# Kernel tuning notes

Hardware: AMD Instinct MI355X
Metric: run time of the kernel (lower is better)

## Reference

```python
import jax, jax.numpy as jnp
import numpy as np

NUM_NODES = 2_000_000
INPUT_DIM = 128
NUM_GRAPHS = 16_384


def setup_inputs() -> dict:
    key = jax.random.key(0)
    k1, k2, k3 = jax.random.split(key, 3)
    x = jax.random.normal(k1, (NUM_NODES, INPUT_DIM), dtype=jnp.float32)
    batch = jnp.sort(jax.random.randint(k2, (NUM_NODES,), 0, NUM_GRAPHS, dtype=jnp.int64))
    # Linear(input_dim, 1) parameters
    W = jax.random.normal(k3, (INPUT_DIM, 1), dtype=jnp.float32) / np.sqrt(INPUT_DIM)
    b = jnp.zeros((1,), dtype=jnp.float32)
    return {"x": x, "batch": batch, "W": W, "b": b}


def reference(x, batch, W, b) -> jnp.ndarray:
    # scores: [N, 1]; softmax over dim=0 (ALL nodes, matching source exactly)
    scores = x @ W + b
    attn = jax.nn.softmax(scores, axis=0)  # [N, 1]
    # weighted features, then scatter-add by graph id (global_add_pool)
    pooled = jax.ops.segment_sum(x * attn, batch, num_segments=NUM_GRAPHS)
    return pooled  # [NUM_GRAPHS, INPUT_DIM]
```

## Files before the change

kernel.cpp:

```cpp
#include <hip/hip_runtime.h>
#include <math.h>

#define N_NODES  2000000
#define DIM      128
#define N_GRAPHS 16384

#define FBLOCKS  2048
#define WAVES    (FBLOCKS * 4)
#define RPW      ((N_NODES + WAVES - 1) / WAVES)

typedef float v4f __attribute__((ext_vector_type(4)));

__global__ __launch_bounds__(256, 8) void fused_kernel(const float* __restrict__ x,
                                                       const int* __restrict__ batch,
                                                       const float* __restrict__ W,
                                                       const float* __restrict__ b,
                                                       float* __restrict__ acc,
                                                       float* __restrict__ blkZ) {
    const int tid  = threadIdx.x;
    const int lane = tid & 63;
    const int l32  = lane & 31;
    const int half = lane >> 5;
    const int wave = blockIdx.x * 4 + (tid >> 6);

    const v4f  wf   = __builtin_nontemporal_load((const v4f*)W + l32);
    const float bias = b[0];

    const int r0 = wave * RPW;
    const int r1 = min(r0 + RPW, N_NODES);

    float zacc = 0.f;

    int r = r0;
    while (r < r1) {
        const int g = batch[r];
        int lo = r + 1, hi = r1;
        while (lo < hi) {
            const int mid = (lo + hi) >> 1;
            if (batch[mid] <= g) lo = mid + 1; else hi = mid;
        }
        const int end = lo;

        v4f racc = {0.f, 0.f, 0.f, 0.f};
        #pragma unroll 4
        for (int rr = r; rr < end; rr += 2) {
            const int row = rr + half;
            if (row < end) {
                const v4f xv = __builtin_nontemporal_load(
                    (const v4f*)(x + (long)row * DIM) + l32);
                float sv = xv[0] * wf[0] + xv[1] * wf[1] + xv[2] * wf[2] + xv[3] * wf[3];
                #pragma unroll
                for (int m = 16; m >= 1; m >>= 1) sv += __shfl_xor(sv, m, 64);
                const float e = __expf(sv + bias);
                zacc += e;
                racc[0] = fmaf(xv[0], e, racc[0]);
                racc[1] = fmaf(xv[1], e, racc[1]);
                racc[2] = fmaf(xv[2], e, racc[2]);
                racc[3] = fmaf(xv[3], e, racc[3]);
            }
        }
        racc[0] += __shfl_xor(racc[0], 32, 64);
        racc[1] += __shfl_xor(racc[1], 32, 64);
        racc[2] += __shfl_xor(racc[2], 32, 64);
        racc[3] += __shfl_xor(racc[3], 32, 64);
        if (half == 0) {
            float* a = acc + (long)g * DIM + l32 * 4;
            atomicAdd(a + 0, racc[0]);
            atomicAdd(a + 1, racc[1]);
            atomicAdd(a + 2, racc[2]);
            atomicAdd(a + 3, racc[3]);
        }
        r = end;
    }

    zacc += __shfl_xor(zacc, 32, 64);
    __shared__ float sm[4];
    if (lane == 0) sm[tid >> 6] = zacc;
    __syncthreads();
    if (tid == 0) blkZ[blockIdx.x] = sm[0] + sm[1] + sm[2] + sm[3];
}

__global__ __launch_bounds__(256) void finalize_kernel(const float* __restrict__ acc,
                                                       const float* __restrict__ blkZ,
                                                       float* __restrict__ out) {
    __shared__ float sm[256];
    float v = 0.f;
    #pragma unroll
    for (int i = 0; i < FBLOCKS / 256; ++i) v += blkZ[i * 256 + threadIdx.x];
    sm[threadIdx.x] = v;
    __syncthreads();
    #pragma unroll
    for (int st = 128; st >= 1; st >>= 1) {
        if (threadIdx.x < st) sm[threadIdx.x] += sm[threadIdx.x + st];
        __syncthreads();
    }
    const float invZ = 1.0f / sm[0];

    const int i = blockIdx.x * 256 + threadIdx.x;
    const float4 a = ((const float4*)acc)[i];
    float4 o;
    o.x = a.x * invZ; o.y = a.y * invZ; o.z = a.z * invZ; o.w = a.w * invZ;
    ((float4*)out)[i] = o;
}

extern "C" void kernel_launch(void* const* d_in, const int* in_sizes, int n_in,
                              void* d_out, int out_size, void* d_ws, size_t ws_size,
                              hipStream_t stream) {
    const float* x     = (const float*)d_in[0];
    const int*   batch = (const int*)d_in[1];
    const float* W     = (const float*)d_in[2];
    const float* b     = (const float*)d_in[3];
    float* out = (float*)d_out;

    float* acc  = (float*)d_ws;
    float* blkZ = acc + (long)N_GRAPHS * DIM;

    hipMemsetAsync(acc, 0, (size_t)N_GRAPHS * DIM * sizeof(float), stream);

    fused_kernel<<<FBLOCKS, 256, 0, stream>>>(x, batch, W, b, acc, blkZ);

    const int fin_grid = (N_GRAPHS * DIM / 4) / 256;
    finalize_kernel<<<fin_grid, 256, 0, stream>>>(acc, blkZ, out);
}
```

Baseline: 196.1 us.

## Assign one wave per graph and drop atomics and memset

Work is now split by graph instead of by equal node ranges. Each wave binary-searches its graph's row range in the sorted batch array, accumulates that graph alone, and writes the result directly to the output. This removes the accumulator memset, the float atomics and the separate accumulator buffer, and the final pass now scales the output in place. In exchange each wave pays two full-array binary searches, and load balance now depends on graph sizes, which are roughly uniform for this input.

```diff
diff --git a/kernel.cpp b/kernel.cpp
--- a/kernel.cpp
+++ b/kernel.cpp
@@ -5,72 +5,65 @@
 #define DIM      128
 #define N_GRAPHS 16384
 
-#define FBLOCKS  2048
-#define WAVES    (FBLOCKS * 4)
-#define RPW      ((N_NODES + WAVES - 1) / WAVES)
+#define GBLOCKS  4096
+#define ZENT     GBLOCKS
 
 typedef float v4f __attribute__((ext_vector_type(4)));
+
+__device__ __forceinline__ int lower_bound(const int* __restrict__ batch, int target) {
+    int lo = 0, hi = N_NODES;
+    while (lo < hi) {
+        const int mid = (lo + hi) >> 1;
+        if (batch[mid] < target) lo = mid + 1; else hi = mid;
+    }
+    return lo;
+}
 
 __global__ __launch_bounds__(256, 8) void fused_kernel(const float* __restrict__ x,
                                                        const int* __restrict__ batch,
                                                        const float* __restrict__ W,
                                                        const float* __restrict__ b,
-                                                       float* __restrict__ acc,
+                                                       float* __restrict__ out,
                                                        float* __restrict__ blkZ) {
     const int tid  = threadIdx.x;
     const int lane = tid & 63;
     const int l32  = lane & 31;
     const int half = lane >> 5;
-    const int wave = blockIdx.x * 4 + (tid >> 6);
+    const int g    = blockIdx.x * 4 + (tid >> 6);
 
-    const v4f  wf   = __builtin_nontemporal_load((const v4f*)W + l32);
+    const v4f wf    = *((const v4f*)W + l32);
     const float bias = b[0];
 
-    const int r0 = wave * RPW;
-    const int r1 = min(r0 + RPW, N_NODES);
+    const int r0 = lower_bound(batch, g);
+    const int r1 = lower_bound(batch, g + 1);
 
     float zacc = 0.f;
+    v4f racc = {0.f, 0.f, 0.f, 0.f};
 
-    int r = r0;
-    while (r < r1) {
-        const int g = batch[r];
-        int lo = r + 1, hi = r1;
-        while (lo < hi) {
-            const int mid = (lo + hi) >> 1;
-            if (batch[mid] <= g) lo = mid + 1; else hi = mid;
+    #pragma unroll 4
+    for (int rr = r0; rr < r1; rr += 2) {
+        const int row = rr + half;
+        if (row < r1) {
+            const v4f xv = __builtin_nontemporal_load(
+                (const v4f*)(x + (long)row * DIM) + l32);
+            float sv = xv[0] * wf[0] + xv[1] * wf[1] + xv[2] * wf[2] + xv[3] * wf[3];
+            #pragma unroll
+            for (int m = 16; m >= 1; m >>= 1) sv += __shfl_xor(sv, m, 64);
+            const float e = __expf(sv + bias);
+            zacc += e;
+            racc[0] = fmaf(xv[0], e, racc[0]);
+            racc[1] = fmaf(xv[1], e, racc[1]);
+            racc[2] = fmaf(xv[2], e, racc[2]);
+            racc[3] = fmaf(xv[3], e, racc[3]);
         }
-        const int end = lo;
+    }
 
-        v4f racc = {0.f, 0.f, 0.f, 0.f};
-        #pragma unroll 4
-        for (int rr = r; rr < end; rr += 2) {
-            const int row = rr + half;
-            if (row < end) {
-                const v4f xv = __builtin_nontemporal_load(
-                    (const v4f*)(x + (long)row * DIM) + l32);
-                float sv = xv[0] * wf[0] + xv[1] * wf[1] + xv[2] * wf[2] + xv[3] * wf[3];
-                #pragma unroll
-                for (int m = 16; m >= 1; m >>= 1) sv += __shfl_xor(sv, m, 64);
-                const float e = __expf(sv + bias);
-                zacc += e;
-                racc[0] = fmaf(xv[0], e, racc[0]);
-                racc[1] = fmaf(xv[1], e, racc[1]);
-                racc[2] = fmaf(xv[2], e, racc[2]);
-                racc[3] = fmaf(xv[3], e, racc[3]);
-            }
-        }
-        racc[0] += __shfl_xor(racc[0], 32, 64);
-        racc[1] += __shfl_xor(racc[1], 32, 64);
-        racc[2] += __shfl_xor(racc[2], 32, 64);
-        racc[3] += __shfl_xor(racc[3], 32, 64);
-        if (half == 0) {
-            float* a = acc + (long)g * DIM + l32 * 4;
-            atomicAdd(a + 0, racc[0]);
-            atomicAdd(a + 1, racc[1]);
-            atomicAdd(a + 2, racc[2]);
-            atomicAdd(a + 3, racc[3]);
-        }
-        r = end;
+    racc[0] += __shfl_xor(racc[0], 32, 64);
+    racc[1] += __shfl_xor(racc[1], 32, 64);
+    racc[2] += __shfl_xor(racc[2], 32, 64);
+    racc[3] += __shfl_xor(racc[3], 32, 64);
+    if (half == 0) {
+        *((v4f*)(out + (long)g * DIM) + l32) = racc;
     }
 
     zacc += __shfl_xor(zacc, 32, 64);
@@ -80,13 +73,12 @@
     if (tid == 0) blkZ[blockIdx.x] = sm[0] + sm[1] + sm[2] + sm[3];
 }
 
-__global__ __launch_bounds__(256) void finalize_kernel(const float* __restrict__ acc,
-                                                       const float* __restrict__ blkZ,
-                                                       float* __restrict__ out) {
+__global__ __launch_bounds__(256) void scale_kernel(float* __restrict__ out,
+                                                    const float* __restrict__ blkZ) {
     __shared__ float sm[256];
     float v = 0.f;
     #pragma unroll
-    for (int i = 0; i < FBLOCKS / 256; ++i) v += blkZ[i * 256 + threadIdx.x];
+    for (int i = 0; i < ZENT / 256; ++i) v += blkZ[i * 256 + threadIdx.x];
     sm[threadIdx.x] = v;
     __syncthreads();
     #pragma unroll
@@ -97,10 +89,9 @@
     const float invZ = 1.0f / sm[0];
 
     const int i = blockIdx.x * 256 + threadIdx.x;
-    const float4 a = ((const float4*)acc)[i];
-    float4 o;
-    o.x = a.x * invZ; o.y = a.y * invZ; o.z = a.z * invZ; o.w = a.w * invZ;
-    ((float4*)out)[i] = o;
+    v4f a = ((v4f*)out)[i];
+    a[0] *= invZ; a[1] *= invZ; a[2] *= invZ; a[3] *= invZ;
+    ((v4f*)out)[i] = a;
 }
 
 extern "C" void kernel_launch(void* const* d_in, const int* in_sizes, int n_in,
@@ -112,13 +103,10 @@
     const float* b     = (const float*)d_in[3];
     float* out = (float*)d_out;
 
-    float* acc  = (float*)d_ws;
-    float* blkZ = acc + (long)N_GRAPHS * DIM;
+    float* blkZ = (float*)d_ws;
 
-    hipMemsetAsync(acc, 0, (size_t)N_GRAPHS * DIM * sizeof(float), stream);
+    fused_kernel<<<GBLOCKS, 256, 0, stream>>>(x, batch, W, b, out, blkZ);
 
-    fused_kernel<<<FBLOCKS, 256, 0, stream>>>(x, batch, W, b, acc, blkZ);
-
-    const int fin_grid = (N_GRAPHS * DIM / 4) / 256;
-    finalize_kernel<<<fin_grid, 256, 0, stream>>>(acc, blkZ, out);
+    const int sc_grid = (N_GRAPHS * DIM / 4) / 256;
+    scale_kernel<<<sc_grid, 256, 0, stream>>>(out, blkZ);
 }
```

New measurement: 208.2 us. 1.06x slower.
